# Kernel tuning notes

Measured on AMD Instinct MI355X. Metric: run time of the kernel, lower is better.

## Reference

```python
import jax, jax.numpy as jnp
import numpy as np
import math

B, S, E, H = 2, 2048, 1024, 16
D = E // H  # head_dim = 64


def setup_inputs() -> dict:
    key = jax.random.key(0)
    ks = jax.random.split(key, 12)
    scale = 1.0 / math.sqrt(E)
    inp = {
        "q": jax.random.normal(ks[0], (B, S, E), jnp.float32),
        "k": jax.random.normal(ks[1], (B, S, E), jnp.float32),
        "v": jax.random.normal(ks[2], (B, S, E), jnp.float32),
        # causal mask, broadcast over batch and heads
        "mask": jnp.tril(jnp.ones((S, S), jnp.bool_))[None, None, :, :],
        "Wq": jax.random.normal(ks[3], (E, E), jnp.float32) * scale,
        "bq": jnp.zeros((E,), jnp.float32),
        "Wk": jax.random.normal(ks[4], (E, E), jnp.float32) * scale,
        "bk": jnp.zeros((E,), jnp.float32),
        "Wv": jax.random.normal(ks[5], (E, E), jnp.float32) * scale,
        "bv": jnp.zeros((E,), jnp.float32),
        "Wo": jax.random.normal(ks[6], (E, E), jnp.float32) * scale,
        "bo": jnp.zeros((E,), jnp.float32),
    }
    return inp


def _heads(x, W, b):
    # nn.Linear: x @ W.T + b, then split into heads -> [B, H, S, D]
    y = x @ W.T + b
    return y.reshape(B, S, H, D).transpose(0, 2, 1, 3)


def reference(q, k, v, mask, Wq, bq, Wk, bk, Wv, bv, Wo, bo):
    qh = _heads(q, Wq, bq)   # [B,H,S,D]
    kh = _heads(k, Wk, bk)
    vh = _heads(v, Wv, bv)
    scores = jnp.einsum("bhqd,bhkd->bhqk", qh, kh) / math.sqrt(D)
    scores = jnp.where(mask, scores, -1e9)
    probs = jax.nn.softmax(scores, axis=-1)  # dropout is identity in eval
    ctx = jnp.einsum("bhqk,bhkd->bhqd", probs, vh)
    ctx = ctx.transpose(0, 2, 1, 3).reshape(B, S, E)
    return ctx @ Wo.T + bo
```

## Files before the change

### kernel.cpp

```cpp
#include <hip/hip_runtime.h>
#include <hip/hip_bf16.h>
#include <cstdint>

#define PB 2
#define PS 2048
#define PE 1024
#define PH 16
#define PD 64

typedef __attribute__((ext_vector_type(8))) short short8;
typedef __attribute__((ext_vector_type(8))) ushort u16x8;
typedef __attribute__((ext_vector_type(4))) float f32x4;

static __device__ __forceinline__ float bf2f(ushort u) {
  return __uint_as_float(((unsigned)u) << 16);
}
static __device__ __forceinline__ ushort f2bf(float f) {
  unsigned u = __float_as_uint(f);
  u += 0x7fffu + ((u >> 16) & 1u);
  return (ushort)(u >> 16);
}
static __device__ __forceinline__ unsigned pkbf(float a, float b) {
  __hip_bfloat162 h = __float22bfloat162_rn(make_float2(a, b));
  return *reinterpret_cast<unsigned*>(&h);
}
static __device__ __forceinline__ u16x8 cvt8(f32x4 a, f32x4 b) {
  union { unsigned u[4]; u16x8 v; } r;
  r.u[0] = pkbf(a[0], a[1]); r.u[1] = pkbf(a[2], a[3]);
  r.u[2] = pkbf(b[0], b[1]); r.u[3] = pkbf(b[2], b[3]);
  return r.v;
}

static __device__ __forceinline__ void async16(void* lds, const void* g) {
  __attribute__((address_space(3))) unsigned* l =
      reinterpret_cast<__attribute__((address_space(3))) unsigned*>(
          reinterpret_cast<uintptr_t>(lds));
  const __attribute__((address_space(1))) unsigned* gp =
      reinterpret_cast<const __attribute__((address_space(1))) unsigned*>(
          reinterpret_cast<uintptr_t>(g));
  __builtin_amdgcn_global_load_lds(gp, l, 16, 0, 0);
}

__global__ __launch_bounds__(256)
void cvt_kernel(const float* __restrict__ s0, const float* __restrict__ s1,
                const float* __restrict__ s2, const float* __restrict__ s3,
                const float* __restrict__ s4, const float* __restrict__ s5,
                const float* __restrict__ s6,
                ushort* d0, ushort* d1, ushort* d2, ushort* d3, ushort* d4,
                ushort* d5, ushort* d6) {
  const int t = blockIdx.y;
  const float* src = t == 0 ? s0 : t == 1 ? s1 : t == 2 ? s2 : t == 3 ? s3
                   : t == 4 ? s4 : t == 5 ? s5 : s6;
  ushort* dst = t == 0 ? d0 : t == 1 ? d1 : t == 2 ? d2 : t == 3 ? d3
              : t == 4 ? d4 : t == 5 ? d5 : d6;
  const size_t n = (t < 3) ? (size_t)4194304 : (size_t)1048576;
  const size_t i0 = ((size_t)blockIdx.x * 256 + threadIdx.x) * 16;
  if (i0 >= n) return;
  const f32x4 a = *(const f32x4*)(src + i0);
  const f32x4 b = *(const f32x4*)(src + i0 + 4);
  const f32x4 c = *(const f32x4*)(src + i0 + 8);
  const f32x4 d = *(const f32x4*)(src + i0 + 12);
  *(u16x8*)(dst + i0) = cvt8(a, b);
  *(u16x8*)(dst + i0 + 8) = cvt8(c, d);
}

template <bool SWAP>
__device__ __forceinline__ void gemm_core(const ushort* __restrict__ A,
                                          const ushort* __restrict__ W,
                                          int m0, int n0,
                                          ushort* As, ushort* Bs,
                                          f32x4 acc[4][4]) {
  const int tid  = threadIdx.x;
  const int wave = tid >> 6;
  const int lane = tid & 63;
  const int quad = lane >> 4;
  const int lrow = lane & 15;
  const int wm = wave >> 1;
  const int wn = wave & 1;
  const int row0 = tid >> 2;
  const int kc8  = (tid & 3) * 8;

  auto stage = [&](int buf, int kt) {
    ushort* Ab = As + buf * 4096;
    ushort* Bb = Bs + buf * 4096;
    async16(Ab + (size_t)wave * 512,        A + (size_t)(m0 + row0)      * PE + kt + kc8);
    async16(Ab + 2048 + (size_t)wave * 512, A + (size_t)(m0 + row0 + 64) * PE + kt + kc8);
    async16(Bb + (size_t)wave * 512,        W + (size_t)(n0 + row0)      * PE + kt + kc8);
    async16(Bb + 2048 + (size_t)wave * 512, W + (size_t)(n0 + row0 + 64) * PE + kt + kc8);
  };

  stage(0, 0);
  __syncthreads();
  int cur = 0;

  for (int kt = 0; kt < PE; kt += 32) {
    if (kt + 32 < PE) stage(cur ^ 1, kt + 32);
    const ushort* Ab = As + cur * 4096;
    const ushort* Bb = Bs + cur * 4096;
    short8 af[4], bf[4];
#pragma unroll
    for (int i = 0; i < 4; ++i) {
      af[i] = *(const short8*)(Ab + (wm * 64 + i * 16 + lrow) * 32 + quad * 8);
      bf[i] = *(const short8*)(Bs + cur * 4096 + (wn * 64 + i * 16 + lrow) * 32 + quad * 8);
    }
    (void)Bb;
#pragma unroll
    for (int i = 0; i < 4; ++i)
#pragma unroll
      for (int j = 0; j < 4; ++j) {
        if (SWAP)
          acc[i][j] = __builtin_amdgcn_mfma_f32_16x16x32_bf16(bf[j], af[i], acc[i][j], 0, 0, 0);
        else
          acc[i][j] = __builtin_amdgcn_mfma_f32_16x16x32_bf16(af[i], bf[j], acc[i][j], 0, 0, 0);
      }
    __syncthreads();
    cur ^= 1;
  }
}

__global__ __launch_bounds__(256)
void qkv_kernel(const ushort* __restrict__ q, const ushort* __restrict__ k,
                const ushort* __restrict__ v,
                const ushort* __restrict__ Wq, const ushort* __restrict__ Wk,
                const ushort* __restrict__ Wv,
                const float* __restrict__ bq, const float* __restrict__ bk,
                const float* __restrict__ bv,
                ushort* __restrict__ qh, ushort* __restrict__ kh,
                ushort* __restrict__ vt) {
  __shared__ __align__(16) ushort As[2 * 128 * 32];
  __shared__ __align__(16) ushort Bs[2 * 128 * 32];
  const int which = blockIdx.y >> 3;
  const int n0 = (blockIdx.y & 7) * 128;
  const int m0 = blockIdx.x * 128;
  const ushort* A  = which == 0 ? q  : (which == 1 ? k  : v);
  const ushort* W  = which == 0 ? Wq : (which == 1 ? Wk : Wv);
  const float* bi  = which == 0 ? bq : (which == 1 ? bk : bv);

  const int lane = threadIdx.x & 63;
  const int wave = threadIdx.x >> 6;
  const int quad = lane >> 4, lrow = lane & 15;
  const int wm = wave >> 1, wn = wave & 1;

  f32x4 acc[4][4] = {};
  if (which == 2) {
    gemm_core<true>(A, W, m0, n0, As, Bs, acc);
#pragma unroll
    for (int j = 0; j < 4; ++j) {
#pragma unroll
      for (int i = 0; i < 4; ++i) {
        const int xrow = m0 + wm * 64 + i * 16 + lrow;
        const int b = xrow >> 11, s = xrow & 2047;
#pragma unroll
        for (int r = 0; r < 4; ++r) {
          const int dcol = n0 + wn * 64 + j * 16 + quad * 4 + r;
          const int h = dcol >> 6, d = dcol & 63;
          vt[((size_t)((b << 4) + h) << 17) + ((size_t)d << 11) + s] =
              f2bf(acc[i][j][r] + bi[dcol]);
        }
      }
    }
  } else {
    gemm_core<false>(A, W, m0, n0, As, Bs, acc);
    ushort* Out = which == 0 ? qh : kh;
#pragma unroll
    for (int j = 0; j < 4; ++j) {
      const int col = n0 + wn * 64 + j * 16 + lrow;
      const float bias = bi[col];
      const int h = col >> 6, d = col & 63;
#pragma unroll
      for (int i = 0; i < 4; ++i)
#pragma unroll
        for (int r = 0; r < 4; ++r) {
          const int row = m0 + wm * 64 + i * 16 + quad * 4 + r;
          const int b = row >> 11, s = row & 2047;
          Out[((size_t)((b << 4) + h) << 17) + ((size_t)s << 6) + d] =
              f2bf(acc[i][j][r] + bias);
        }
    }
  }
}

__global__ __launch_bounds__(256)
void outproj_kernel(const ushort* __restrict__ ctx, const ushort* __restrict__ Wo,
                    const float* __restrict__ bo, float* __restrict__ out) {
  __shared__ __align__(16) ushort As[2 * 128 * 32];
  __shared__ __align__(16) ushort Bs[2 * 128 * 32];
  const int n0 = blockIdx.y * 128;
  const int m0 = blockIdx.x * 128;

  f32x4 acc[4][4] = {};
  gemm_core<false>(ctx, Wo, m0, n0, As, Bs, acc);

  const int lane = threadIdx.x & 63;
  const int wave = threadIdx.x >> 6;
  const int quad = lane >> 4, lrow = lane & 15;
  const int wm = wave >> 1, wn = wave & 1;
#pragma unroll
  for (int j = 0; j < 4; ++j) {
    const int col = n0 + wn * 64 + j * 16 + lrow;
    const float bias = bo[col];
#pragma unroll
    for (int i = 0; i < 4; ++i)
#pragma unroll
      for (int r = 0; r < 4; ++r) {
        const int row = m0 + wm * 64 + i * 16 + quad * 4 + r;
        out[((size_t)row << 10) + col] = acc[i][j][r] + bias;
      }
  }
}

#define SW_IDX(r, g) (((r) << 6) + ((((g) ^ ((r) & 7))) << 3))
#define QSCALE 0.180336879f
#define SOFF 24.0f

__global__ __launch_bounds__(256)
void attn_kernel(const ushort* __restrict__ qh, const ushort* __restrict__ kh,
                 const ushort* __restrict__ vt, ushort* __restrict__ ctx) {
  __shared__ __align__(16) ushort Ks[2][4096];
  __shared__ __align__(16) ushort Vs[2][4096];
  __shared__ __align__(16) ushort Ps[4][1024];
  const int tid  = threadIdx.x;
  const int wave = tid >> 6;
  const int lane = tid & 63;
  const int quad = lane >> 4;
  const int lrow = lane & 15;
  const int bh = blockIdx.x, b = bh >> 4, h = bh & 15;
  const size_t base = (size_t)bh << 17;
  const int srow = tid >> 2;
  const int sg0  = (tid & 3) * 2;
  const int pr   = wave * 16 + lrow;
  ushort* Pw = &Ps[wave][0];
  const int prow = lrow << 6;

  const int y  = blockIdx.y;
  const int qb = (y < 8) ? 31 - y : (y < 16) ? y - 8 : (y < 24) ? 39 - y : y - 16;
  const int q0 = qb * 64;

  short8 qf0, qf1;
  {
    const ushort* qp = qh + base + (size_t)(q0 + pr) * 64 + quad * 8;
    const u16x8 a = *(const u16x8*)qp;
    const u16x8 c = *(const u16x8*)(qp + 32);
#pragma unroll
    for (int j = 0; j < 8; ++j) {
      qf0[j] = (short)f2bf(bf2f(a[j]) * QSCALE);
      qf1[j] = (short)f2bf(bf2f(c[j]) * QSCALE);
    }
  }

  short8 ones;
#pragma unroll
  for (int j = 0; j < 8; ++j) ones[j] = (short)0x3F80;

  f32x4 o_acc[4] = {};
  f32x4 lacc = {};

  u16x8 kst0, kst1, vst0, vst1;
  {
    const ushort* kp = kh + base + (size_t)srow * 64 + sg0 * 8;
    kst0 = *(const u16x8*)kp; kst1 = *(const u16x8*)(kp + 8);
    const ushort* vp = vt + base + (size_t)srow * 2048 + sg0 * 8;
    vst0 = *(const u16x8*)vp; vst1 = *(const u16x8*)(vp + 8);
  }

  for (int kt = 0; kt <= qb; ++kt) {
    const int buf = kt & 1;
    *(u16x8*)&Ks[buf][SW_IDX(srow, sg0)]     = kst0;
    *(u16x8*)&Ks[buf][SW_IDX(srow, sg0 + 1)] = kst1;
    *(u16x8*)&Vs[buf][SW_IDX(srow, sg0)]     = vst0;
    *(u16x8*)&Vs[buf][SW_IDX(srow, sg0 + 1)] = vst1;
    __syncthreads();

    if (kt < qb) {
      const ushort* kp = kh + base + (size_t)((kt + 1) * 64 + srow) * 64 + sg0 * 8;
      kst0 = *(const u16x8*)kp; kst1 = *(const u16x8*)(kp + 8);
      const ushort* vp = vt + base + (size_t)srow * 2048 + (kt + 1) * 64 + sg0 * 8;
      vst0 = *(const u16x8*)vp; vst1 = *(const u16x8*)(vp + 8);
    }

    f32x4 st[4];
#pragma unroll
    for (int nt = 0; nt < 4; ++nt) {
      const int r = nt * 16 + lrow;
      const short8 kb0 = *(const short8*)&Ks[buf][SW_IDX(r, quad)];
      const short8 kb1 = *(const short8*)&Ks[buf][SW_IDX(r, quad + 4)];
      st[nt] = (f32x4){-SOFF, -SOFF, -SOFF, -SOFF};
      st[nt] = __builtin_amdgcn_mfma_f32_16x16x32_bf16(kb0, qf0, st[nt], 0, 0, 0);
      st[nt] = __builtin_amdgcn_mfma_f32_16x16x32_bf16(kb1, qf1, st[nt], 0, 0, 0);
    }

    if (kt == qb) {
#pragma unroll
      for (int nt = 0; nt < 4; ++nt)
#pragma unroll
        for (int r = 0; r < 4; ++r)
          if (nt * 16 + quad * 4 + r > pr) st[nt][r] = -1e30f;
    }

#pragma unroll
    for (int nt = 0; nt < 4; ++nt) {
      float p0 = exp2f(st[nt][0]);
      float p1 = exp2f(st[nt][1]);
      float p2 = exp2f(st[nt][2]);
      float p3 = exp2f(st[nt][3]);
      uint2 pk;
      pk.x = pkbf(p0, p1); pk.y = pkbf(p2, p3);
      *(uint2*)&Pw[prow + (((nt * 2 + (quad >> 1)) ^ (lrow & 7)) << 3) +
                   (quad & 1) * 4] = pk;
    }

    const short8 pa0 = *(const short8*)&Pw[prow + ((quad ^ (lrow & 7)) << 3)];
    const short8 pa1 = *(const short8*)&Pw[prow + (((quad + 4) ^ (lrow & 7)) << 3)];
    lacc = __builtin_amdgcn_mfma_f32_16x16x32_bf16(ones, pa0, lacc, 0, 0, 0);
    lacc = __builtin_amdgcn_mfma_f32_16x16x32_bf16(ones, pa1, lacc, 0, 0, 0);
#pragma unroll
    for (int nt = 0; nt < 4; ++nt) {
      const int r = nt * 16 + lrow;
      const short8 vb0 = *(const short8*)&Vs[buf][SW_IDX(r, quad)];
      const short8 vb1 = *(const short8*)&Vs[buf][SW_IDX(r, quad + 4)];
      o_acc[nt] = __builtin_amdgcn_mfma_f32_16x16x32_bf16(vb0, pa0, o_acc[nt], 0, 0, 0);
      o_acc[nt] = __builtin_amdgcn_mfma_f32_16x16x32_bf16(vb1, pa1, o_acc[nt], 0, 0, 0);
    }
  }

  const float inv = 1.f / lacc[0];
  const size_t rowb = ((size_t)b << 21) + ((size_t)(q0 + pr) << 10) + (h << 6);
#pragma unroll
  for (int nt = 0; nt < 4; ++nt) {
    uint2 u;
    u.x = pkbf(o_acc[nt][0] * inv, o_acc[nt][1] * inv);
    u.y = pkbf(o_acc[nt][2] * inv, o_acc[nt][3] * inv);
    *(uint2*)(ctx + rowb + nt * 16 + quad * 4) = u;
  }
}

extern "C" void kernel_launch(void* const* d_in, const int* in_sizes, int n_in,
                              void* d_out, int out_size, void* d_ws, size_t ws_size,
                              hipStream_t stream) {
  const float* q  = (const float*)d_in[0];
  const float* k  = (const float*)d_in[1];
  const float* v  = (const float*)d_in[2];
  const float* Wq = (const float*)d_in[4];
  const float* bq = (const float*)d_in[5];
  const float* Wk = (const float*)d_in[6];
  const float* bk = (const float*)d_in[7];
  const float* Wv = (const float*)d_in[8];
  const float* bv = (const float*)d_in[9];
  const float* Wo = (const float*)d_in[10];
  const float* bo = (const float*)d_in[11];

  const size_t NTOK = (size_t)PB * PS * PE;
  const size_t NW   = (size_t)PE * PE;
  ushort* qh  = (ushort*)d_ws;
  ushort* kh  = qh + NTOK;
  ushort* vt  = kh + NTOK;
  ushort* qc  = vt + NTOK;
  ushort* kc  = qc + NTOK;
  ushort* vc  = kc + NTOK;
  ushort* wqc = vc + NTOK;
  ushort* wkc = wqc + NW;
  ushort* wvc = wkc + NW;
  ushort* woc = wvc + NW;
  ushort* ctx = qc;

  cvt_kernel<<<dim3(1024, 7), dim3(256), 0, stream>>>(
      q, k, v, Wq, Wk, Wv, Wo, qc, kc, vc, wqc, wkc, wvc, woc);
  qkv_kernel<<<dim3(32, 24), dim3(256), 0, stream>>>(
      qc, kc, vc, wqc, wkc, wvc, bq, bk, bv, qh, kh, vt);
  attn_kernel<<<dim3(32, 32), dim3(256), 0, stream>>>(qh, kh, vt, ctx);
  outproj_kernel<<<dim3(32, 8), dim3(256), 0, stream>>>(
      ctx, woc, bo, (float*)d_out);
}
```

Baseline: 218.6 us.

## Load K/V fragments straight from global memory and remap attention blocks per XCD

The attention kernel drops its double-buffered LDS staging of K and V tiles and the per-tile __syncthreads. Each wave now reads its MFMA operands directly from global memory, relying on L2 caching since all four waves read the same tile. The grid is flattened to 1D and remapped so that every (batch, head) pair's query blocks land on the same XCD, which should improve L2 reuse of K/V. The cost is redundant global loads across waves and no explicit prefetch, so load latency is exposed on each tile.

```diff
diff --git a/kernel.cpp b/kernel.cpp
--- a/kernel.cpp
+++ b/kernel.cpp
@@ -96,14 +96,12 @@
   for (int kt = 0; kt < PE; kt += 32) {
     if (kt + 32 < PE) stage(cur ^ 1, kt + 32);
     const ushort* Ab = As + cur * 4096;
-    const ushort* Bb = Bs + cur * 4096;
     short8 af[4], bf[4];
 #pragma unroll
     for (int i = 0; i < 4; ++i) {
       af[i] = *(const short8*)(Ab + (wm * 64 + i * 16 + lrow) * 32 + quad * 8);
       bf[i] = *(const short8*)(Bs + cur * 4096 + (wn * 64 + i * 16 + lrow) * 32 + quad * 8);
     }
-    (void)Bb;
 #pragma unroll
     for (int i = 0; i < 4; ++i)
 #pragma unroll
@@ -209,31 +207,31 @@
   }
 }
 
-#define SW_IDX(r, g) (((r) << 6) + ((((g) ^ ((r) & 7))) << 3))
 #define QSCALE 0.180336879f
 #define SOFF 24.0f
 
 __global__ __launch_bounds__(256)
 void attn_kernel(const ushort* __restrict__ qh, const ushort* __restrict__ kh,
                  const ushort* __restrict__ vt, ushort* __restrict__ ctx) {
-  __shared__ __align__(16) ushort Ks[2][4096];
-  __shared__ __align__(16) ushort Vs[2][4096];
   __shared__ __align__(16) ushort Ps[4][1024];
   const int tid  = threadIdx.x;
   const int wave = tid >> 6;
   const int lane = tid & 63;
   const int quad = lane >> 4;
   const int lrow = lane & 15;
-  const int bh = blockIdx.x, b = bh >> 4, h = bh & 15;
+
+  const int id   = blockIdx.x;
+  const int xcd  = id & 7;
+  const int slot = id >> 3;
+  const int bh   = (xcd << 2) | (slot & 3);
+  const int g    = slot >> 2;
+  const int qb   = (g < 8) ? 31 - g : (g < 16) ? g - 8 : (g < 24) ? 39 - g
+                                                                  : g - 16;
+  const int b = bh >> 4, h = bh & 15;
   const size_t base = (size_t)bh << 17;
-  const int srow = tid >> 2;
-  const int sg0  = (tid & 3) * 2;
   const int pr   = wave * 16 + lrow;
   ushort* Pw = &Ps[wave][0];
   const int prow = lrow << 6;
-
-  const int y  = blockIdx.y;
-  const int qb = (y < 8) ? 31 - y : (y < 16) ? y - 8 : (y < 24) ? 39 - y : y - 16;
   const int q0 = qb * 64;
 
   short8 qf0, qf1;
@@ -255,35 +253,14 @@
   f32x4 o_acc[4] = {};
   f32x4 lacc = {};
 
-  u16x8 kst0, kst1, vst0, vst1;
-  {
-    const ushort* kp = kh + base + (size_t)srow * 64 + sg0 * 8;
-    kst0 = *(const u16x8*)kp; kst1 = *(const u16x8*)(kp + 8);
-    const ushort* vp = vt + base + (size_t)srow * 2048 + sg0 * 8;
-    vst0 = *(const u16x8*)vp; vst1 = *(const u16x8*)(vp + 8);
-  }
-
   for (int kt = 0; kt <= qb; ++kt) {
-    const int buf = kt & 1;
-    *(u16x8*)&Ks[buf][SW_IDX(srow, sg0)]     = kst0;
-    *(u16x8*)&Ks[buf][SW_IDX(srow, sg0 + 1)] = kst1;
-    *(u16x8*)&Vs[buf][SW_IDX(srow, sg0)]     = vst0;
-    *(u16x8*)&Vs[buf][SW_IDX(srow, sg0 + 1)] = vst1;
-    __syncthreads();
-
-    if (kt < qb) {
-      const ushort* kp = kh + base + (size_t)((kt + 1) * 64 + srow) * 64 + sg0 * 8;
-      kst0 = *(const u16x8*)kp; kst1 = *(const u16x8*)(kp + 8);
-      const ushort* vp = vt + base + (size_t)srow * 2048 + (kt + 1) * 64 + sg0 * 8;
-      vst0 = *(const u16x8*)vp; vst1 = *(const u16x8*)(vp + 8);
-    }
-
+    const ushort* kbase = kh + base + ((size_t)kt << 12);
     f32x4 st[4];
 #pragma unroll
     for (int nt = 0; nt < 4; ++nt) {
       const int r = nt * 16 + lrow;
-      const short8 kb0 = *(const short8*)&Ks[buf][SW_IDX(r, quad)];
-      const short8 kb1 = *(const short8*)&Ks[buf][SW_IDX(r, quad + 4)];
+      const short8 kb0 = *(const short8*)(kbase + r * 64 + quad * 8);
+      const short8 kb1 = *(const short8*)(kbase + r * 64 + quad * 8 + 32);
       st[nt] = (f32x4){-SOFF, -SOFF, -SOFF, -SOFF};
       st[nt] = __builtin_amdgcn_mfma_f32_16x16x32_bf16(kb0, qf0, st[nt], 0, 0, 0);
       st[nt] = __builtin_amdgcn_mfma_f32_16x16x32_bf16(kb1, qf1, st[nt], 0, 0, 0);
@@ -313,11 +290,13 @@
     const short8 pa1 = *(const short8*)&Pw[prow + (((quad + 4) ^ (lrow & 7)) << 3)];
     lacc = __builtin_amdgcn_mfma_f32_16x16x32_bf16(ones, pa0, lacc, 0, 0, 0);
     lacc = __builtin_amdgcn_mfma_f32_16x16x32_bf16(ones, pa1, lacc, 0, 0, 0);
+
+    const ushort* vbase = vt + base + kt * 64;
 #pragma unroll
     for (int nt = 0; nt < 4; ++nt) {
       const int r = nt * 16 + lrow;
-      const short8 vb0 = *(const short8*)&Vs[buf][SW_IDX(r, quad)];
-      const short8 vb1 = *(const short8*)&Vs[buf][SW_IDX(r, quad + 4)];
+      const short8 vb0 = *(const short8*)(vbase + (size_t)r * 2048 + quad * 8);
+      const short8 vb1 = *(const short8*)(vbase + (size_t)r * 2048 + quad * 8 + 32);
       o_acc[nt] = __builtin_amdgcn_mfma_f32_16x16x32_bf16(vb0, pa0, o_acc[nt], 0, 0, 0);
       o_acc[nt] = __builtin_amdgcn_mfma_f32_16x16x32_bf16(vb1, pa1, o_acc[nt], 0, 0, 0);
     }
@@ -367,7 +346,7 @@
       q, k, v, Wq, Wk, Wv, Wo, qc, kc, vc, wqc, wkc, wvc, woc);
   qkv_kernel<<<dim3(32, 24), dim3(256), 0, stream>>>(
       qc, kc, vc, wqc, wkc, wvc, bq, bk, bv, qh, kh, vt);
-  attn_kernel<<<dim3(32, 32), dim3(256), 0, stream>>>(qh, kh, vt, ctx);
+  attn_kernel<<<dim3(1024), dim3(256), 0, stream>>>(qh, kh, vt, ctx);
   outproj_kernel<<<dim3(32, 8), dim3(256), 0, stream>>>(
       ctx, woc, bo, (float*)d_out);
 }
```

After: 305.7 us. +39.8%, slower.

## Split attention keys across waves and keep P in registers with cross-wave reduction

Applied to the files above, without the earlier changes.

The attention kernel now has each wave own 16 key columns of every 64-key tile, computing scores for all 64 query rows, instead of each wave owning 16 query rows. P stays in registers and is fed straight into the PV MFMA by pairing two consecutive key tiles, using a triple-buffered V tile. This removes the per-wave P round trip through shared memory. In exchange it needs a final cross-wave reduction of O and the row sums through shared memory, and more accumulator registers (16 O tiles per wave). It also drops an unused variable in the GEMM.

```diff
diff --git a/kernel.cpp b/kernel.cpp
--- a/kernel.cpp
+++ b/kernel.cpp
@@ -96,14 +96,12 @@
   for (int kt = 0; kt < PE; kt += 32) {
     if (kt + 32 < PE) stage(cur ^ 1, kt + 32);
     const ushort* Ab = As + cur * 4096;
-    const ushort* Bb = Bs + cur * 4096;
     short8 af[4], bf[4];
 #pragma unroll
     for (int i = 0; i < 4; ++i) {
       af[i] = *(const short8*)(Ab + (wm * 64 + i * 16 + lrow) * 32 + quad * 8);
       bf[i] = *(const short8*)(Bs + cur * 4096 + (wn * 64 + i * 16 + lrow) * 32 + quad * 8);
     }
-    (void)Bb;
 #pragma unroll
     for (int i = 0; i < 4; ++i)
 #pragma unroll
@@ -216,9 +214,9 @@
 __global__ __launch_bounds__(256)
 void attn_kernel(const ushort* __restrict__ qh, const ushort* __restrict__ kh,
                  const ushort* __restrict__ vt, ushort* __restrict__ ctx) {
-  __shared__ __align__(16) ushort Ks[2][4096];
-  __shared__ __align__(16) ushort Vs[2][4096];
-  __shared__ __align__(16) ushort Ps[4][1024];
+  __shared__ __align__(16) ushort SMEM[20480];
+  ushort* Ks = SMEM;
+  ushort* Vs = SMEM + 8192;
   const int tid  = threadIdx.x;
   const int wave = tid >> 6;
   const int lane = tid & 63;
@@ -229,22 +227,22 @@
   const int srow = tid >> 2;
   const int sg0  = (tid & 3) * 2;
   const int pr   = wave * 16 + lrow;
-  ushort* Pw = &Ps[wave][0];
-  const int prow = lrow << 6;
+  const int w16  = wave * 16;
 
   const int y  = blockIdx.y;
   const int qb = (y < 8) ? 31 - y : (y < 16) ? y - 8 : (y < 24) ? 39 - y : y - 16;
   const int q0 = qb * 64;
 
-  short8 qf0, qf1;
-  {
-    const ushort* qp = qh + base + (size_t)(q0 + pr) * 64 + quad * 8;
+  short8 qf[4][2];
+#pragma unroll
+  for (int ct = 0; ct < 4; ++ct) {
+    const ushort* qp = qh + base + (size_t)(q0 + ct * 16 + lrow) * 64 + quad * 8;
     const u16x8 a = *(const u16x8*)qp;
     const u16x8 c = *(const u16x8*)(qp + 32);
 #pragma unroll
     for (int j = 0; j < 8; ++j) {
-      qf0[j] = (short)f2bf(bf2f(a[j]) * QSCALE);
-      qf1[j] = (short)f2bf(bf2f(c[j]) * QSCALE);
+      qf[ct][0][j] = (short)f2bf(bf2f(a[j]) * QSCALE);
+      qf[ct][1][j] = (short)f2bf(bf2f(c[j]) * QSCALE);
     }
   }
 
@@ -252,8 +250,8 @@
 #pragma unroll
   for (int j = 0; j < 8; ++j) ones[j] = (short)0x3F80;
 
-  f32x4 o_acc[4] = {};
-  f32x4 lacc = {};
+  f32x4 o_acc[4][4] = {};
+  f32x4 lacc[4] = {};
 
   u16x8 kst0, kst1, vst0, vst1;
   {
@@ -263,12 +261,37 @@
     vst0 = *(const u16x8*)vp; vst1 = *(const u16x8*)(vp + 8);
   }
 
+  uint2 pkA[4];
+  int vbuf = 0, vprev = 0;
+
+  auto do_pv = [&](const ushort* VA, const ushort* VB,
+                   const uint2* A, const uint2* B) {
+#pragma unroll
+    for (int ct = 0; ct < 4; ++ct) {
+      union { unsigned u[4]; short8 v; } pb;
+      pb.u[0] = A[ct].x; pb.u[1] = A[ct].y;
+      pb.u[2] = B[ct].x; pb.u[3] = B[ct].y;
+      lacc[ct] = __builtin_amdgcn_mfma_f32_16x16x32_bf16(ones, pb.v, lacc[ct], 0, 0, 0);
+#pragma unroll
+      for (int dt = 0; dt < 4; ++dt) {
+        const int row = dt * 16 + lrow;
+        const int off = (row << 6) +
+                        (((w16 >> 3) + (quad >> 1) ^ (row & 7)) << 3) +
+                        ((quad & 1) << 2);
+        union { uint2 u2[2]; short8 v; } va;
+        va.u2[0] = *(const uint2*)(VA + off);
+        va.u2[1] = *(const uint2*)(VB + off);
+        o_acc[dt][ct] = __builtin_amdgcn_mfma_f32_16x16x32_bf16(va.v, pb.v, o_acc[dt][ct], 0, 0, 0);
+      }
+    }
+  };
+
   for (int kt = 0; kt <= qb; ++kt) {
-    const int buf = kt & 1;
-    *(u16x8*)&Ks[buf][SW_IDX(srow, sg0)]     = kst0;
-    *(u16x8*)&Ks[buf][SW_IDX(srow, sg0 + 1)] = kst1;
-    *(u16x8*)&Vs[buf][SW_IDX(srow, sg0)]     = vst0;
-    *(u16x8*)&Vs[buf][SW_IDX(srow, sg0 + 1)] = vst1;
+    const int kbuf = kt & 1;
+    *(u16x8*)&Ks[kbuf * 4096 + SW_IDX(srow, sg0)]     = kst0;
+    *(u16x8*)&Ks[kbuf * 4096 + SW_IDX(srow, sg0 + 1)] = kst1;
+    *(u16x8*)&Vs[vbuf * 4096 + SW_IDX(srow, sg0)]     = vst0;
+    *(u16x8*)&Vs[vbuf * 4096 + SW_IDX(srow, sg0 + 1)] = vst1;
     __syncthreads();
 
     if (kt < qb) {
@@ -278,58 +301,86 @@
       vst0 = *(const u16x8*)vp; vst1 = *(const u16x8*)(vp + 8);
     }
 
+    const ushort* Kb = Ks + kbuf * 4096;
+    const short8 kb0 = *(const short8*)&Kb[SW_IDX(w16 + lrow, quad)];
+    const short8 kb1 = *(const short8*)&Kb[SW_IDX(w16 + lrow, quad + 4)];
     f32x4 st[4];
 #pragma unroll
-    for (int nt = 0; nt < 4; ++nt) {
-      const int r = nt * 16 + lrow;
-      const short8 kb0 = *(const short8*)&Ks[buf][SW_IDX(r, quad)];
-      const short8 kb1 = *(const short8*)&Ks[buf][SW_IDX(r, quad + 4)];
-      st[nt] = (f32x4){-SOFF, -SOFF, -SOFF, -SOFF};
-      st[nt] = __builtin_amdgcn_mfma_f32_16x16x32_bf16(kb0, qf0, st[nt], 0, 0, 0);
-      st[nt] = __builtin_amdgcn_mfma_f32_16x16x32_bf16(kb1, qf1, st[nt], 0, 0, 0);
+    for (int ct = 0; ct < 4; ++ct) {
+      st[ct] = (f32x4){-SOFF, -SOFF, -SOFF, -SOFF};
+      st[ct] = __builtin_amdgcn_mfma_f32_16x16x32_bf16(kb0, qf[ct][0], st[ct], 0, 0, 0);
+      st[ct] = __builtin_amdgcn_mfma_f32_16x16x32_bf16(kb1, qf[ct][1], st[ct], 0, 0, 0);
     }
 
     if (kt == qb) {
 #pragma unroll
-      for (int nt = 0; nt < 4; ++nt)
+      for (int ct = 0; ct < 4; ++ct)
 #pragma unroll
         for (int r = 0; r < 4; ++r)
-          if (nt * 16 + quad * 4 + r > pr) st[nt][r] = -1e30f;
-    }
-
-#pragma unroll
-    for (int nt = 0; nt < 4; ++nt) {
-      float p0 = exp2f(st[nt][0]);
-      float p1 = exp2f(st[nt][1]);
-      float p2 = exp2f(st[nt][2]);
-      float p3 = exp2f(st[nt][3]);
-      uint2 pk;
-      pk.x = pkbf(p0, p1); pk.y = pkbf(p2, p3);
-      *(uint2*)&Pw[prow + (((nt * 2 + (quad >> 1)) ^ (lrow & 7)) << 3) +
-                   (quad & 1) * 4] = pk;
-    }
-
-    const short8 pa0 = *(const short8*)&Pw[prow + ((quad ^ (lrow & 7)) << 3)];
-    const short8 pa1 = *(const short8*)&Pw[prow + (((quad + 4) ^ (lrow & 7)) << 3)];
-    lacc = __builtin_amdgcn_mfma_f32_16x16x32_bf16(ones, pa0, lacc, 0, 0, 0);
-    lacc = __builtin_amdgcn_mfma_f32_16x16x32_bf16(ones, pa1, lacc, 0, 0, 0);
-#pragma unroll
-    for (int nt = 0; nt < 4; ++nt) {
-      const int r = nt * 16 + lrow;
-      const short8 vb0 = *(const short8*)&Vs[buf][SW_IDX(r, quad)];
-      const short8 vb1 = *(const short8*)&Vs[buf][SW_IDX(r, quad + 4)];
-      o_acc[nt] = __builtin_amdgcn_mfma_f32_16x16x32_bf16(vb0, pa0, o_acc[nt], 0, 0, 0);
-      o_acc[nt] = __builtin_amdgcn_mfma_f32_16x16x32_bf16(vb1, pa1, o_acc[nt], 0, 0, 0);
-    }
-  }
-
-  const float inv = 1.f / lacc[0];
+          if (w16 + quad * 4 + r > ct * 16 + lrow) st[ct][r] = -1e30f;
+    }
+
+    uint2 pcur[4];
+#pragma unroll
+    for (int ct = 0; ct < 4; ++ct) {
+      const float p0 = exp2f(st[ct][0]);
+      const float p1 = exp2f(st[ct][1]);
+      const float p2 = exp2f(st[ct][2]);
+      const float p3 = exp2f(st[ct][3]);
+      pcur[ct].x = pkbf(p0, p1); pcur[ct].y = pkbf(p2, p3);
+    }
+
+    if ((kt & 1) == 0) {
+#pragma unroll
+      for (int ct = 0; ct < 4; ++ct) pkA[ct] = pcur[ct];
+      vprev = vbuf;
+    } else {
+      do_pv(Vs + vprev * 4096, Vs + vbuf * 4096, pkA, pcur);
+    }
+    vbuf = (vbuf == 2) ? 0 : vbuf + 1;
+  }
+
+  if ((qb & 1) == 0) {
+    uint2 z[4];
+#pragma unroll
+    for (int ct = 0; ct < 4; ++ct) { z[ct].x = 0u; z[ct].y = 0u; }
+    do_pv(Vs + vprev * 4096, Vs + vprev * 4096, pkA, z);
+  }
+
+  __syncthreads();
+  float* Ored = (float*)SMEM;
+  float* Lred = (float*)SMEM + 64 * 68;
+  if (quad == 0) {
+#pragma unroll
+    for (int ct = 0; ct < 4; ++ct)
+      Lred[wave * 64 + ct * 16 + lrow] = lacc[ct][0];
+  }
+#pragma unroll
+  for (int p = 0; p < 4; ++p) {
+    const int ct = (wave + p) & 3;
+#pragma unroll
+    for (int dt = 0; dt < 4; ++dt) {
+      float* pos = Ored + (ct * 16 + lrow) * 68 + dt * 16 + quad * 4;
+      if (p == 0) {
+        *(f32x4*)pos = o_acc[dt][ct];
+      } else {
+        f32x4 c = *(const f32x4*)pos;
+        c += o_acc[dt][ct];
+        *(f32x4*)pos = c;
+      }
+    }
+    __syncthreads();
+  }
+
+  const float l = Lred[pr] + Lred[64 + pr] + Lred[128 + pr] + Lred[192 + pr];
+  const float inv = 1.f / l;
   const size_t rowb = ((size_t)b << 21) + ((size_t)(q0 + pr) << 10) + (h << 6);
 #pragma unroll
   for (int nt = 0; nt < 4; ++nt) {
+    const f32x4 o = *(const f32x4*)(Ored + pr * 68 + nt * 16 + quad * 4);
     uint2 u;
-    u.x = pkbf(o_acc[nt][0] * inv, o_acc[nt][1] * inv);
-    u.y = pkbf(o_acc[nt][2] * inv, o_acc[nt][3] * inv);
+    u.x = pkbf(o[0] * inv, o[1] * inv);
+    u.y = pkbf(o[2] * inv, o[3] * inv);
     *(uint2*)(ctx + rowb + nt * 16 + quad * 4) = u;
   }
 }
```

Measured after the change: 386.3 us. 1.77x slower.

## Use async direct-to-LDS K/V staging with wave priority hints in attention

Applied to the files above, without the earlier changes.

The attention kernel now loads K and V tiles with async global-to-LDS copies into a double buffer, prefetching the next tile before computing the current one. This replaces the register-staged loads and explicit LDS stores, and moves the barrier to the end of each iteration. It also raises wave priority around the MFMA blocks with s_setprio so matrix work is issued ahead of other waves. The swizzle is now applied on the global-address side, and correctness depends on the async copies completing before the barrier. A dead variable in the GEMM loop is also removed.

```diff
diff --git a/kernel.cpp b/kernel.cpp
--- a/kernel.cpp
+++ b/kernel.cpp
@@ -96,14 +96,12 @@
   for (int kt = 0; kt < PE; kt += 32) {
     if (kt + 32 < PE) stage(cur ^ 1, kt + 32);
     const ushort* Ab = As + cur * 4096;
-    const ushort* Bb = Bs + cur * 4096;
     short8 af[4], bf[4];
 #pragma unroll
     for (int i = 0; i < 4; ++i) {
       af[i] = *(const short8*)(Ab + (wm * 64 + i * 16 + lrow) * 32 + quad * 8);
       bf[i] = *(const short8*)(Bs + cur * 4096 + (wn * 64 + i * 16 + lrow) * 32 + quad * 8);
     }
-    (void)Bb;
 #pragma unroll
     for (int i = 0; i < 4; ++i)
 #pragma unroll
@@ -226,8 +224,6 @@
   const int lrow = lane & 15;
   const int bh = blockIdx.x, b = bh >> 4, h = bh & 15;
   const size_t base = (size_t)bh << 17;
-  const int srow = tid >> 2;
-  const int sg0  = (tid & 3) * 2;
   const int pr   = wave * 16 + lrow;
   ushort* Pw = &Ps[wave][0];
   const int prow = lrow << 6;
@@ -235,6 +231,20 @@
   const int y  = blockIdx.y;
   const int qb = (y < 8) ? 31 - y : (y < 16) ? y - 8 : (y < 24) ? 39 - y : y - 16;
   const int q0 = qb * 64;
+
+  const int w16  = wave * 16;
+  const int rl   = lane >> 3;
+  const int gsw  = ((lane & 7) ^ rl) << 3;
+  auto stageKV = [&](int buf, int kt) {
+    const ushort* k0 = kh + base + (size_t)(kt * 64 + w16 + rl) * 64 + gsw;
+    const ushort* k1 = kh + base + (size_t)(kt * 64 + w16 + 8 + rl) * 64 + gsw;
+    async16(&Ks[buf][w16 << 6],       k0);
+    async16(&Ks[buf][(w16 + 8) << 6], k1);
+    const ushort* v0 = vt + base + (size_t)(w16 + rl) * 2048 + kt * 64 + gsw;
+    const ushort* v1 = vt + base + (size_t)(w16 + 8 + rl) * 2048 + kt * 64 + gsw;
+    async16(&Vs[buf][w16 << 6],       v0);
+    async16(&Vs[buf][(w16 + 8) << 6], v1);
+  };
 
   short8 qf0, qf1;
   {
@@ -255,30 +265,15 @@
   f32x4 o_acc[4] = {};
   f32x4 lacc = {};
 
-  u16x8 kst0, kst1, vst0, vst1;
-  {
-    const ushort* kp = kh + base + (size_t)srow * 64 + sg0 * 8;
-    kst0 = *(const u16x8*)kp; kst1 = *(const u16x8*)(kp + 8);
-    const ushort* vp = vt + base + (size_t)srow * 2048 + sg0 * 8;
-    vst0 = *(const u16x8*)vp; vst1 = *(const u16x8*)(vp + 8);
-  }
+  stageKV(0, 0);
+  __syncthreads();
 
   for (int kt = 0; kt <= qb; ++kt) {
     const int buf = kt & 1;
-    *(u16x8*)&Ks[buf][SW_IDX(srow, sg0)]     = kst0;
-    *(u16x8*)&Ks[buf][SW_IDX(srow, sg0 + 1)] = kst1;
-    *(u16x8*)&Vs[buf][SW_IDX(srow, sg0)]     = vst0;
-    *(u16x8*)&Vs[buf][SW_IDX(srow, sg0 + 1)] = vst1;
-    __syncthreads();
-
-    if (kt < qb) {
-      const ushort* kp = kh + base + (size_t)((kt + 1) * 64 + srow) * 64 + sg0 * 8;
-      kst0 = *(const u16x8*)kp; kst1 = *(const u16x8*)(kp + 8);
-      const ushort* vp = vt + base + (size_t)srow * 2048 + (kt + 1) * 64 + sg0 * 8;
-      vst0 = *(const u16x8*)vp; vst1 = *(const u16x8*)(vp + 8);
-    }
+    if (kt < qb) stageKV(buf ^ 1, kt + 1);
 
     f32x4 st[4];
+    __builtin_amdgcn_s_setprio(1);
 #pragma unroll
     for (int nt = 0; nt < 4; ++nt) {
       const int r = nt * 16 + lrow;
@@ -288,6 +283,7 @@
       st[nt] = __builtin_amdgcn_mfma_f32_16x16x32_bf16(kb0, qf0, st[nt], 0, 0, 0);
       st[nt] = __builtin_amdgcn_mfma_f32_16x16x32_bf16(kb1, qf1, st[nt], 0, 0, 0);
     }
+    __builtin_amdgcn_s_setprio(0);
 
     if (kt == qb) {
 #pragma unroll
@@ -311,6 +307,7 @@
 
     const short8 pa0 = *(const short8*)&Pw[prow + ((quad ^ (lrow & 7)) << 3)];
     const short8 pa1 = *(const short8*)&Pw[prow + (((quad + 4) ^ (lrow & 7)) << 3)];
+    __builtin_amdgcn_s_setprio(1);
     lacc = __builtin_amdgcn_mfma_f32_16x16x32_bf16(ones, pa0, lacc, 0, 0, 0);
     lacc = __builtin_amdgcn_mfma_f32_16x16x32_bf16(ones, pa1, lacc, 0, 0, 0);
 #pragma unroll
@@ -321,6 +318,8 @@
       o_acc[nt] = __builtin_amdgcn_mfma_f32_16x16x32_bf16(vb0, pa0, o_acc[nt], 0, 0, 0);
       o_acc[nt] = __builtin_amdgcn_mfma_f32_16x16x32_bf16(vb1, pa1, o_acc[nt], 0, 0, 0);
     }
+    __builtin_amdgcn_s_setprio(0);
+    __syncthreads();
   }
 
   const float inv = 1.f / lacc[0];
```

New measurement: 217.3 us. About the same (-0.6%).
